# Optimization experiments

Hardware: AMD Instinct MI355X
Metric: run time of the kernel (lower is better)

Reference implementation:

```python
import jax, jax.numpy as jnp
import numpy as np

TILE = 64        # tile_hw -> P = TILE*TILE = 4096 rays per image
N_GAUSS = 16384
N_CAMS = 8
N_IMGS = 2
EPS = 1e-5


def setup_inputs() -> dict:
    key = jax.random.key(0)
    k1, k2, k3, k4, k5, k6 = jax.random.split(key, 6)
    means = jax.random.normal(k1, (N_GAUSS, 3), dtype=jnp.float32)
    # covariances only used through their diagonal mean; keep diagonals positive
    covs = jax.random.uniform(k2, (N_GAUSS, 3, 3), dtype=jnp.float32, minval=0.05, maxval=1.0)
    colors = jax.random.uniform(k3, (N_GAUSS, 3), dtype=jnp.float32)
    fx = fy = 70.0
    cx = cy = TILE / 2.0
    intrinsics = jnp.tile(jnp.array([fx, fy, cx, cy], dtype=jnp.float32), (N_CAMS, 1))
    # extrinsics: identity rotation, camera ~4 units along +z with jitter, looking toward -z
    trans = jnp.concatenate(
        [0.5 * jax.random.normal(k4, (N_CAMS, 2)),
         4.0 + 0.2 * jax.random.normal(k5, (N_CAMS, 1))], axis=-1).astype(jnp.float32)
    extrinsics = jnp.broadcast_to(jnp.eye(4, dtype=jnp.float32), (N_CAMS, 4, 4))
    extrinsics = extrinsics.at[:, :3, 3].set(trans)
    image_ids = jax.random.randint(k6, (N_IMGS,), 0, N_CAMS)
    return {"means": means, "covs": covs, "colors": colors,
            "intrinsics": intrinsics, "extrinsics": extrinsics, "image_ids": image_ids}


def _render_one(means, covs, colors, intr, c2w):
    fx, fy, cx, cy = intr[0], intr[1], intr[2], intr[3]
    # ray generation (matches torch meshgrid indexing='xy')
    i, j = jnp.meshgrid(jnp.arange(TILE, dtype=jnp.float32),
                        jnp.arange(TILE, dtype=jnp.float32), indexing='xy')
    dirs = jnp.stack([(i - cx) / fx, -(j - cy) / fy, -jnp.ones_like(i)], axis=-1)  # [H,W,3]
    Rrot = c2w[:3, :3]
    rays_d = jnp.einsum('hwk,jk->hwj', dirs, Rrot).reshape(-1, 3)   # [P,3] = dirs @ R^T
    rays_o = jnp.broadcast_to(c2w[:3, 3], rays_d.shape)             # [P,3]

    # per-ray gaussian distance weights (attention-like score)
    diff = means[None, :, :] - rays_o[:, None, :]                   # [P,N,3]
    t = jnp.sum(diff * rays_d[:, None, :], axis=-1, keepdims=True)  # [P,N,1]
    closest = rays_o[:, None, :] + rays_d[:, None, :] * t           # [P,N,3]
    pdiff = means[None, :, :] - closest                             # [P,N,3]
    sigma = jnp.sqrt(jnp.mean(jnp.diagonal(covs, axis1=1, axis2=2), axis=1))  # [N]
    dist2 = jnp.sum(pdiff ** 2, axis=-1)                            # [P,N]
    weights = jnp.exp(-0.5 * dist2 / (sigma[None, :] ** 2 + EPS))   # [P,N]

    # weighted color aggregation + normalization (softmax-like value aggregation)
    rgb = (weights @ colors) / (jnp.sum(weights, axis=-1, keepdims=True) + EPS)  # [P,3]
    return rgb.T.reshape(3, TILE * TILE)


def reference(means, covs, colors, intrinsics, extrinsics, image_ids):
    cam_i = intrinsics[image_ids]   # [B,4]
    cam_e = extrinsics[image_ids]   # [B,4,4]
    render = lambda intr, c2w: _render_one(means, covs, colors, intr, c2w)
    return jax.vmap(render)(cam_i, cam_e)   # [B, 3, TILE*TILE]
```

## Files before the change

### kernel.cpp

```cpp
#include <hip/hip_runtime.h>

#define N_GAUSS 16384
#define SPLIT   64
#define GPS     (N_GAUSS / SPLIT)
#define TILE    64
#define NPIX    (TILE * TILE)
#define EPS     1e-5f
#define LOG2E   1.44269504088896340736f

__global__ void precompute_kernel(const float* __restrict__ means,
                                  const float* __restrict__ covs,
                                  const float* __restrict__ colors,
                                  const float* __restrict__ extr,
                                  const int*   __restrict__ img_ids,
                                  float4* __restrict__ AB,
                                  int n_imgs) {
    int idx = blockIdx.x * blockDim.x + threadIdx.x;
    if (idx >= n_imgs * N_GAUSS) return;
    const int img = idx / N_GAUSS;
    const int g   = idx - img * N_GAUSS;

    const float mx = means[3 * g + 0];
    const float my = means[3 * g + 1];
    const float mz = means[3 * g + 2];
    const float* c = covs + 9 * g;
    const float s2  = (c[0] + c[4] + c[8]) * (1.0f / 3.0f);
    const float sig = sqrtf(s2);
    const float kg2 = -0.5f * LOG2E / (sig * sig + EPS);

    const int cam = img_ids[img];
    const float* E = extr + 16 * cam;
    const float ox = E[3], oy = E[7], oz = E[11];
    const float ux = mx - ox, uy = my - oy, uz = mz - oz;
    const float n2c = ux * ux + uy * uy + uz * uz;

    AB[2 * idx + 0] = make_float4(mx, my, mz, kg2);
    AB[2 * idx + 1] = make_float4(colors[3 * g + 0], colors[3 * g + 1],
                                  colors[3 * g + 2], kg2 * n2c);
}

__global__ __launch_bounds__(256, 8) void render_kernel(
        const float4* __restrict__ AB,
        const float*  __restrict__ intr,
        const float*  __restrict__ extr,
        const int*    __restrict__ img_ids,
        float4*       __restrict__ partial,
        int n_imgs) {
    const int tid   = threadIdx.x;
    const int split = blockIdx.y;
    const int img   = blockIdx.z;

    const int cam = img_ids[img];
    const float* I = intr + 4 * cam;
    const float* E = extr + 16 * cam;
    const float fx = I[0], fy = I[1], cx = I[2], cy = I[3];

    const int pixel = blockIdx.x * 256 + tid;
    const int row = pixel >> 6;
    const int col = pixel & 63;

    const float d0 = ((float)col - cx) / fx;
    const float d1 = -(((float)row) - cy) / fy;
    const float d2 = -1.0f;
    const float rdx = d0 * E[0] + d1 * E[1] + d2 * E[2];
    const float rdy = d0 * E[4] + d1 * E[5] + d2 * E[6];
    const float rdz = d0 * E[8] + d1 * E[9] + d2 * E[10];
    const float ox = E[3], oy = E[7], oz = E[11];

    const float dd2 = rdx * rdx + rdy * rdy + rdz * rdz - 2.0f;
    const float mod = -(ox * rdx + oy * rdy + oz * rdz);

    const float4* __restrict__ base = AB + 2 * (img * N_GAUSS + split * GPS);

    float wsum = 0.0f, cr = 0.0f, cg = 0.0f, cb = 0.0f;
    #pragma unroll 8
    for (int g = 0; g < GPS; g++) {
        const float4 a = base[2 * g + 0];
        const float4 b = base[2 * g + 1];
        const float t  = fmaf(a.x, rdx, fmaf(a.y, rdy, fmaf(a.z, rdz, mod)));
        const float q  = a.w * (t * t);
        const float w  = __builtin_amdgcn_exp2f(fmaf(q, dd2, b.w));
        wsum += w;
        cr = fmaf(w, b.x, cr);
        cg = fmaf(w, b.y, cg);
        cb = fmaf(w, b.z, cb);
    }

    const int idx = img * NPIX + pixel;
    partial[split * (n_imgs * NPIX) + idx] = make_float4(wsum, cr, cg, cb);
}

__global__ void reduce_kernel(const float4* __restrict__ partial,
                              float* __restrict__ out,
                              int n_imgs) {
    const int idx = blockIdx.x * blockDim.x + threadIdx.x;
    const int total = n_imgs * NPIX;
    if (idx >= total) return;
    float w = 0.0f, r = 0.0f, g = 0.0f, b = 0.0f;
    #pragma unroll 8
    for (int s = 0; s < SPLIT; s++) {
        const float4 p = partial[s * total + idx];
        w += p.x; r += p.y; g += p.z; b += p.w;
    }
    const float inv = 1.0f / (w + EPS);
    const int img = idx >> 12;
    const int pix = idx & (NPIX - 1);
    out[(img * 3 + 0) * NPIX + pix] = r * inv;
    out[(img * 3 + 1) * NPIX + pix] = g * inv;
    out[(img * 3 + 2) * NPIX + pix] = b * inv;
}

extern "C" void kernel_launch(void* const* d_in, const int* in_sizes, int n_in,
                              void* d_out, int out_size, void* d_ws, size_t ws_size,
                              hipStream_t stream) {
    const float* means   = (const float*)d_in[0];
    const float* covs    = (const float*)d_in[1];
    const float* colors  = (const float*)d_in[2];
    const float* intr    = (const float*)d_in[3];
    const float* extr    = (const float*)d_in[4];
    const int*   img_ids = (const int*)d_in[5];
    float* out = (float*)d_out;
    const int n_imgs = in_sizes[5];

    float4* AB      = (float4*)d_ws;
    float4* partial = AB + 2 * n_imgs * N_GAUSS;

    const int npre = n_imgs * N_GAUSS;
    precompute_kernel<<<(npre + 255) / 256, 256, 0, stream>>>(
        means, covs, colors, extr, img_ids, AB, n_imgs);

    dim3 grid(NPIX / 256, SPLIT, n_imgs);
    render_kernel<<<grid, 256, 0, stream>>>(AB, intr, extr, img_ids, partial, n_imgs);

    const int total = n_imgs * NPIX;
    reduce_kernel<<<(total + 255) / 256, 256, 0, stream>>>(partial, out, n_imgs);
}
```

Before: 117.0 us.

## Fuse precompute into render via LDS staging, two pixels per thread, atomic accumulation

Drops the separate precompute kernel: each block computes its slice of per-gaussian constants straight into shared memory. The exponent is refactored so that scaled ray vectors and sqrt(-kg2) turn the quadratic into a single square plus an offset. Each thread now handles two pixels so every LDS read is shared across two rays. The partial buffer and 64-way reduction are replaced by float atomicAdd into a zeroed accumulator and a small finalize pass. The trade-off is atomic contention across 128 splits, non-deterministic summation order, and an extra memset.

```diff
diff --git a/kernel.cpp b/kernel.cpp
--- a/kernel.cpp
+++ b/kernel.cpp
@@ -1,113 +1,110 @@
 #include <hip/hip_runtime.h>
 
 #define N_GAUSS 16384
-#define SPLIT   64
+#define SPLIT   128
 #define GPS     (N_GAUSS / SPLIT)
 #define TILE    64
 #define NPIX    (TILE * TILE)
+#define PPT     2
 #define EPS     1e-5f
 #define LOG2E   1.44269504088896340736f
 
-__global__ void precompute_kernel(const float* __restrict__ means,
-                                  const float* __restrict__ covs,
-                                  const float* __restrict__ colors,
-                                  const float* __restrict__ extr,
-                                  const int*   __restrict__ img_ids,
-                                  float4* __restrict__ AB,
-                                  int n_imgs) {
-    int idx = blockIdx.x * blockDim.x + threadIdx.x;
-    if (idx >= n_imgs * N_GAUSS) return;
-    const int img = idx / N_GAUSS;
-    const int g   = idx - img * N_GAUSS;
+__global__ __launch_bounds__(256, 8) void render_kernel(
+        const float* __restrict__ means,
+        const float* __restrict__ covs,
+        const float* __restrict__ colors,
+        const float* __restrict__ intr,
+        const float* __restrict__ extr,
+        const int*   __restrict__ img_ids,
+        float*       __restrict__ acc) {
+    __shared__ float4 sA[GPS];
+    __shared__ float4 sB[GPS];
 
-    const float mx = means[3 * g + 0];
-    const float my = means[3 * g + 1];
-    const float mz = means[3 * g + 2];
-    const float* c = covs + 9 * g;
-    const float s2  = (c[0] + c[4] + c[8]) * (1.0f / 3.0f);
-    const float sig = sqrtf(s2);
-    const float kg2 = -0.5f * LOG2E / (sig * sig + EPS);
-
-    const int cam = img_ids[img];
-    const float* E = extr + 16 * cam;
-    const float ox = E[3], oy = E[7], oz = E[11];
-    const float ux = mx - ox, uy = my - oy, uz = mz - oz;
-    const float n2c = ux * ux + uy * uy + uz * uz;
-
-    AB[2 * idx + 0] = make_float4(mx, my, mz, kg2);
-    AB[2 * idx + 1] = make_float4(colors[3 * g + 0], colors[3 * g + 1],
-                                  colors[3 * g + 2], kg2 * n2c);
-}
-
-__global__ __launch_bounds__(256, 8) void render_kernel(
-        const float4* __restrict__ AB,
-        const float*  __restrict__ intr,
-        const float*  __restrict__ extr,
-        const int*    __restrict__ img_ids,
-        float4*       __restrict__ partial,
-        int n_imgs) {
     const int tid   = threadIdx.x;
     const int split = blockIdx.y;
     const int img   = blockIdx.z;
 
     const int cam = img_ids[img];
+    const float* E = extr + 16 * cam;
+    const float ox = E[3], oy = E[7], oz = E[11];
+
+    if (tid < GPS) {
+        const int g = split * GPS + tid;
+        const float mx = means[3 * g + 0];
+        const float my = means[3 * g + 1];
+        const float mz = means[3 * g + 2];
+        const float* c = covs + 9 * g;
+        const float s2  = (c[0] + c[4] + c[8]) * (1.0f / 3.0f);
+        const float sig = sqrtf(s2);
+        const float kg2 = -0.5f * LOG2E / (sig * sig + EPS);
+        const float sg  = sqrtf(-kg2);
+        const float ux = mx - ox, uy = my - oy, uz = mz - oz;
+        const float e0 = kg2 * (ux * ux + uy * uy + uz * uz);
+        sA[tid] = make_float4(mx, my, mz, sg);
+        sB[tid] = make_float4(colors[3 * g + 0], colors[3 * g + 1],
+                              colors[3 * g + 2], e0);
+    }
+
     const float* I = intr + 4 * cam;
-    const float* E = extr + 16 * cam;
     const float fx = I[0], fy = I[1], cx = I[2], cy = I[3];
 
-    const int pixel = blockIdx.x * 256 + tid;
-    const int row = pixel >> 6;
-    const int col = pixel & 63;
-
-    const float d0 = ((float)col - cx) / fx;
-    const float d1 = -(((float)row) - cy) / fy;
-    const float d2 = -1.0f;
-    const float rdx = d0 * E[0] + d1 * E[1] + d2 * E[2];
-    const float rdy = d0 * E[4] + d1 * E[5] + d2 * E[6];
-    const float rdz = d0 * E[8] + d1 * E[9] + d2 * E[10];
-    const float ox = E[3], oy = E[7], oz = E[11];
-
-    const float dd2 = rdx * rdx + rdy * rdy + rdz * rdz - 2.0f;
-    const float mod = -(ox * rdx + oy * rdy + oz * rdz);
-
-    const float4* __restrict__ base = AB + 2 * (img * N_GAUSS + split * GPS);
-
-    float wsum = 0.0f, cr = 0.0f, cg = 0.0f, cb = 0.0f;
-    #pragma unroll 8
-    for (int g = 0; g < GPS; g++) {
-        const float4 a = base[2 * g + 0];
-        const float4 b = base[2 * g + 1];
-        const float t  = fmaf(a.x, rdx, fmaf(a.y, rdy, fmaf(a.z, rdz, mod)));
-        const float q  = a.w * (t * t);
-        const float w  = __builtin_amdgcn_exp2f(fmaf(q, dd2, b.w));
-        wsum += w;
-        cr = fmaf(w, b.x, cr);
-        cg = fmaf(w, b.y, cg);
-        cb = fmaf(w, b.z, cb);
+    float rdx[PPT], rdy[PPT], rdz[PPT], mods[PPT];
+    int pix[PPT];
+    #pragma unroll
+    for (int p = 0; p < PPT; p++) {
+        pix[p] = blockIdx.x * 256 + tid + p * (NPIX / PPT);
+        const int row = pix[p] >> 6;
+        const int col = pix[p] & 63;
+        const float d0 = ((float)col - cx) / fx;
+        const float d1 = -(((float)row) - cy) / fy;
+        const float d2 = -1.0f;
+        const float x = d0 * E[0] + d1 * E[1] + d2 * E[2];
+        const float y = d0 * E[4] + d1 * E[5] + d2 * E[6];
+        const float z = d0 * E[8] + d1 * E[9] + d2 * E[10];
+        const float dd2 = x * x + y * y + z * z - 2.0f;
+        const float sp  = sqrtf(-dd2);
+        rdx[p] = x * sp; rdy[p] = y * sp; rdz[p] = z * sp;
+        mods[p] = -(ox * x + oy * y + oz * z) * sp;
     }
 
-    const int idx = img * NPIX + pixel;
-    partial[split * (n_imgs * NPIX) + idx] = make_float4(wsum, cr, cg, cb);
+    __syncthreads();
+
+    float w0 = 0.f, r0 = 0.f, g0 = 0.f, b0 = 0.f;
+    float w1 = 0.f, r1 = 0.f, g1 = 0.f, b1 = 0.f;
+    #pragma unroll 4
+    for (int g = 0; g < GPS; g++) {
+        const float4 a = sA[g];
+        const float4 b = sB[g];
+        const float t0 = fmaf(a.x, rdx[0], fmaf(a.y, rdy[0], fmaf(a.z, rdz[0], mods[0])));
+        const float t1 = fmaf(a.x, rdx[1], fmaf(a.y, rdy[1], fmaf(a.z, rdz[1], mods[1])));
+        const float u0 = t0 * a.w;
+        const float u1 = t1 * a.w;
+        const float e_0 = __builtin_amdgcn_exp2f(fmaf(u0, u0, b.w));
+        const float e_1 = __builtin_amdgcn_exp2f(fmaf(u1, u1, b.w));
+        w0 += e_0; r0 = fmaf(e_0, b.x, r0); g0 = fmaf(e_0, b.y, g0); b0 = fmaf(e_0, b.z, b0);
+        w1 += e_1; r1 = fmaf(e_1, b.x, r1); g1 = fmaf(e_1, b.y, g1); b1 = fmaf(e_1, b.z, b1);
+    }
+
+    float* A0 = acc + 4 * (img * NPIX + pix[0]);
+    atomicAdd(A0 + 0, w0); atomicAdd(A0 + 1, r0);
+    atomicAdd(A0 + 2, g0); atomicAdd(A0 + 3, b0);
+    float* A1 = acc + 4 * (img * NPIX + pix[1]);
+    atomicAdd(A1 + 0, w1); atomicAdd(A1 + 1, r1);
+    atomicAdd(A1 + 2, g1); atomicAdd(A1 + 3, b1);
 }
 
-__global__ void reduce_kernel(const float4* __restrict__ partial,
-                              float* __restrict__ out,
-                              int n_imgs) {
+__global__ void finalize_kernel(const float4* __restrict__ acc,
+                                float* __restrict__ out,
+                                int n_imgs) {
     const int idx = blockIdx.x * blockDim.x + threadIdx.x;
-    const int total = n_imgs * NPIX;
-    if (idx >= total) return;
-    float w = 0.0f, r = 0.0f, g = 0.0f, b = 0.0f;
-    #pragma unroll 8
-    for (int s = 0; s < SPLIT; s++) {
-        const float4 p = partial[s * total + idx];
-        w += p.x; r += p.y; g += p.z; b += p.w;
-    }
-    const float inv = 1.0f / (w + EPS);
+    if (idx >= n_imgs * NPIX) return;
+    const float4 p = acc[idx];
+    const float inv = 1.0f / (p.x + EPS);
     const int img = idx >> 12;
     const int pix = idx & (NPIX - 1);
-    out[(img * 3 + 0) * NPIX + pix] = r * inv;
-    out[(img * 3 + 1) * NPIX + pix] = g * inv;
-    out[(img * 3 + 2) * NPIX + pix] = b * inv;
+    out[(img * 3 + 0) * NPIX + pix] = p.y * inv;
+    out[(img * 3 + 1) * NPIX + pix] = p.z * inv;
+    out[(img * 3 + 2) * NPIX + pix] = p.w * inv;
 }
 
 extern "C" void kernel_launch(void* const* d_in, const int* in_sizes, int n_in,
@@ -122,16 +119,14 @@
     float* out = (float*)d_out;
     const int n_imgs = in_sizes[5];
 
-    float4* AB      = (float4*)d_ws;
-    float4* partial = AB + 2 * n_imgs * N_GAUSS;
+    float* acc = (float*)d_ws;
+    hipMemsetAsync(acc, 0, (size_t)n_imgs * NPIX * 4 * sizeof(float), stream);
 
-    const int npre = n_imgs * N_GAUSS;
-    precompute_kernel<<<(npre + 255) / 256, 256, 0, stream>>>(
-        means, covs, colors, extr, img_ids, AB, n_imgs);
-
-    dim3 grid(NPIX / 256, SPLIT, n_imgs);
-    render_kernel<<<grid, 256, 0, stream>>>(AB, intr, extr, img_ids, partial, n_imgs);
+    dim3 grid(NPIX / (256 * PPT), SPLIT, n_imgs);
+    render_kernel<<<grid, 256, 0, stream>>>(means, covs, colors, intr, extr,
+                                            img_ids, acc);
 
     const int total = n_imgs * NPIX;
-    reduce_kernel<<<(total + 255) / 256, 256, 0, stream>>>(partial, out, n_imgs);
+    finalize_kernel<<<(total + 255) / 256, 256, 0, stream>>>(
+        (const float4*)acc, out, n_imgs);
 }
```

Result: slower. 148.5 us (+26.9%).
